# Kernel optimization log

Measured on AMD Instinct MI355X. Metric: run time of the kernel, lower is better.

## Reference

```python
import jax, jax.numpy as jnp
import numpy as np

D_QK = 32  # out_channels // 8


def conv1x1(x, w, b):
    # x: [B,C,H,W], w: [O,C], b: [O] -> [B,O,H,W]
    return jnp.einsum('bchw,oc->bohw', x, w) + b[None, :, None, None]


def setup_inputs() -> dict:
    key = jax.random.key(0)
    ks = jax.random.split(key, 10)
    B, C, H, W = 4, 256, 64, 64
    in_ch, out_ch, attn_ch = 512, 256, 256
    s_in = 1.0 / np.sqrt(in_ch)
    s_at = 1.0 / np.sqrt(attn_ch)
    return {
        'ef': jax.random.normal(ks[0], (B, C, H, W), jnp.float32),
        'sf': jax.random.normal(ks[1], (B, C, H, W), jnp.float32),
        'Attn': jax.random.normal(ks[2], (B, attn_ch, H, W), jnp.float32),
        'Qw': jax.random.uniform(ks[3], (D_QK, in_ch), jnp.float32, -s_in, s_in),
        'Qb': jax.random.uniform(ks[4], (D_QK,), jnp.float32, -s_in, s_in),
        'Kw': jax.random.uniform(ks[5], (D_QK, attn_ch), jnp.float32, -s_at, s_at),
        'Kb': jax.random.uniform(ks[6], (D_QK,), jnp.float32, -s_at, s_at),
        'Vw': jax.random.uniform(ks[7], (out_ch, in_ch), jnp.float32, -s_in, s_in),
        'Vb': jax.random.uniform(ks[8], (out_ch,), jnp.float32, -s_in, s_in),
        'gamma': jnp.ones((1,), jnp.float32) * 0.25,
    }


def reference(ef, sf, Attn, Qw, Qb, Kw, Kb, Vw, Vb, gamma):
    B, C, H, W = ef.shape
    N = H * W
    x = jnp.concatenate((ef, sf), axis=1)  # [B, 2C, H, W]
    q = conv1x1(x, Qw, Qb).reshape(B, D_QK, N)         # [B, d, N]
    k = conv1x1(Attn, Kw, Kb).reshape(B, D_QK, N)      # [B, d, N]
    # scores[b, m, n] = sum_d q[b, d, m] * k[b, d, n]  (no 1/sqrt(d) scale)
    scores = jnp.einsum('bdm,bdn->bmn', q, k)
    attn = jax.nn.softmax(scores, axis=-1)             # [B, N, N]
    v = conv1x1(x, Vw, Vb).reshape(B, C, N)            # [B, C, N]
    # out[b, c, m] = sum_n v[b, c, n] * attn[b, m, n]
    out = jnp.einsum('bcn,bmn->bcm', v, attn).reshape(B, C, H, W)
    return gamma[0] * out + ef
```

## Files before the change

kernel.cpp:

```cpp
#include <hip/hip_runtime.h>
#include <hip/hip_bf16.h>

typedef short bf16x8 __attribute__((ext_vector_type(8)));
typedef float f32x4 __attribute__((ext_vector_type(4)));

#define MFMA16(a, b, c) __builtin_amdgcn_mfma_f32_16x16x32_bf16(a, b, c, 0, 0, 0)

#define NB 4
#define NC 256
#define NSP 4096
#define LOG2E 1.4426950408889634f

__device__ __forceinline__ unsigned short f2bf(float f) {
    return (unsigned short)((__float_as_uint(f) + 0x8000u) >> 16);
}
__device__ __forceinline__ unsigned pk2bf(float hi, float lo) {
    return __builtin_amdgcn_perm(__float_as_uint(hi) + 0x8000u,
                                 __float_as_uint(lo) + 0x8000u, 0x07060302u);
}

__global__ __launch_bounds__(256) void prep_w(
    const float* __restrict__ Qw, const float* __restrict__ Kw,
    const float* __restrict__ Vw,
    unsigned short* __restrict__ Qwbf, unsigned short* __restrict__ Kwbf,
    unsigned short* __restrict__ Vwbf)
{
    int i = blockIdx.x * 256 + threadIdx.x;
    {
        const float4* vs = (const float4*)(Vw + (size_t)i * 8);
        float4 a = vs[0], c = vs[1];
        int4 st;
        st.x = (int)pk2bf(a.y, a.x); st.y = (int)pk2bf(a.w, a.z);
        st.z = (int)pk2bf(c.y, c.x); st.w = (int)pk2bf(c.w, c.z);
        *(int4*)(Vwbf + (size_t)i * 8) = st;
    }
    if (i < 2048) {
        const float4* qs = (const float4*)(Qw + (size_t)i * 8);
        float4 a = qs[0], c = qs[1];
        int4 st;
        st.x = (int)pk2bf(a.y, a.x); st.y = (int)pk2bf(a.w, a.z);
        st.z = (int)pk2bf(c.y, c.x); st.w = (int)pk2bf(c.w, c.z);
        *(int4*)(Qwbf + (size_t)i * 8) = st;
    }
    if (i < 1024) {
        const float4* ks = (const float4*)(Kw + (size_t)i * 8);
        float4 a = ks[0], c = ks[1];
        int4 st;
        st.x = (int)pk2bf(a.y, a.x); st.y = (int)pk2bf(a.w, a.z);
        st.z = (int)pk2bf(c.y, c.x); st.w = (int)pk2bf(c.w, c.z);
        *(int4*)(Kwbf + (size_t)i * 8) = st;
    }
}

__global__ __launch_bounds__(256, 2) void proj_qv(
    const float* __restrict__ ef, const float* __restrict__ sf,
    const unsigned short* __restrict__ Qwbf, const float* __restrict__ Qb,
    const unsigned short* __restrict__ Vwbf, const float* __restrict__ Vb,
    unsigned short* __restrict__ qws, unsigned short* __restrict__ vws)
{
    __shared__ __align__(16) unsigned short xt[2][32][72];

    int t = threadIdx.x;
    int w = t >> 6, lane = t & 63, quad = lane >> 4, l15 = lane & 15;
    int mt = blockIdx.x, b = blockIdx.y, m0 = mt * 32;
    int u = t & 7, v = t >> 3;
    int mi = w >> 1, oh = w & 1;

    float4 xA[8], xB[8];
#pragma unroll
    for (int c = 0; c < 8; ++c) {
        const float* sp = (c < 4 ? ef : sf) +
                          ((size_t)(b * NC) + (c & 3) * 64 + 2 * v) * NSP + m0 + u * 4;
        xA[c] = *(const float4*)sp;
        xB[c] = *(const float4*)(sp + NSP);
    }
    __builtin_amdgcn_sched_barrier(0);

    f32x4 zero = {0.f, 0.f, 0.f, 0.f};
    f32x4 acc[2][4];
#pragma unroll
    for (int m = 0; m < 2; ++m)
#pragma unroll
        for (int ot = 0; ot < 4; ++ot) acc[m][ot] = zero;
    f32x4 qacc = zero;

#pragma unroll
    for (int c = 0; c < 8; ++c) {
        unsigned* xw = (unsigned*)&xt[c & 1][u * 4][2 * v];
        xw[0]   = pk2bf(xB[c].x, xA[c].x);
        xw[36]  = pk2bf(xB[c].y, xA[c].y);
        xw[72]  = pk2bf(xB[c].z, xA[c].z);
        xw[108] = pk2bf(xB[c].w, xA[c].w);
        __syncthreads();
        int ci0 = c * 64;
#pragma unroll
        for (int ks = 0; ks < 2; ++ks) {
            bf16x8 a0 = *(const bf16x8*)&xt[c & 1][l15][ks * 32 + quad * 8];
            bf16x8 a1 = *(const bf16x8*)&xt[c & 1][16 + l15][ks * 32 + quad * 8];
            bf16x8 bq = *(const bf16x8*)(Qwbf + (size_t)(oh * 16 + l15) * 512 + ci0 + ks * 32 + quad * 8);
            qacc = MFMA16(mi ? a1 : a0, bq, qacc);
#pragma unroll
            for (int ot = 0; ot < 4; ++ot) {
                bf16x8 bv = *(const bf16x8*)(Vwbf + (size_t)(w * 64 + ot * 16 + l15) * 512 + ci0 + ks * 32 + quad * 8);
                acc[0][ot] = MFMA16(a0, bv, acc[0][ot]);
                acc[1][ot] = MFMA16(a1, bv, acc[1][ot]);
            }
        }
    }

#pragma unroll
    for (int ot = 0; ot < 4; ++ot) {
        int ch = w * 64 + ot * 16 + l15;
        float bias = Vb[ch];
        unsigned* vp = (unsigned*)(vws + ((size_t)((b * 128 + mt) * 256 + ch)) * 32);
#pragma unroll
        for (int r = 0; r < 4; ++r)
            vp[quad * 4 + r] = pk2bf(acc[1][ot][r] + bias, acc[0][ot][r] + bias);
    }
    {
        int o = oh * 16 + l15;
        float bb = Qb[o];
#pragma unroll
        for (int r = 0; r < 4; ++r) {
            int m = m0 + mi * 16 + quad * 4 + r;
            qws[((size_t)(b * NSP) + m) * 32 + o] = f2bf((qacc[r] + bb) * LOG2E);
        }
    }
}

__global__ __launch_bounds__(256, 2) void proj_k(
    const float* __restrict__ attn,
    const unsigned short* __restrict__ Kwbf, const float* __restrict__ Kb,
    unsigned short* __restrict__ kws)
{
    __shared__ __align__(16) unsigned short xt[2][32][72];

    int t = threadIdx.x;
    int w = t >> 6, lane = t & 63, quad = lane >> 4, l15 = lane & 15;
    int mt = blockIdx.x, b = blockIdx.y, m0 = mt * 32;
    int u = t & 7, v = t >> 3;
    int mi = w >> 1, oh = w & 1;

    float4 xA[4], xB[4];
#pragma unroll
    for (int c = 0; c < 4; ++c) {
        const float* sp = attn + ((size_t)(b * NC) + c * 64 + 2 * v) * NSP + m0 + u * 4;
        xA[c] = *(const float4*)sp;
        xB[c] = *(const float4*)(sp + NSP);
    }
    __builtin_amdgcn_sched_barrier(0);

    f32x4 acc = {0.f, 0.f, 0.f, 0.f};

#pragma unroll
    for (int c = 0; c < 4; ++c) {
        unsigned* xw = (unsigned*)&xt[c & 1][u * 4][2 * v];
        xw[0]   = pk2bf(xB[c].x, xA[c].x);
        xw[36]  = pk2bf(xB[c].y, xA[c].y);
        xw[72]  = pk2bf(xB[c].z, xA[c].z);
        xw[108] = pk2bf(xB[c].w, xA[c].w);
        __syncthreads();
        int ci0 = c * 64;
#pragma unroll
        for (int ks = 0; ks < 2; ++ks) {
            bf16x8 a  = *(const bf16x8*)&xt[c & 1][mi * 16 + l15][ks * 32 + quad * 8];
            bf16x8 bk = *(const bf16x8*)(Kwbf + (size_t)(oh * 16 + l15) * 256 + ci0 + ks * 32 + quad * 8);
            acc = MFMA16(a, bk, acc);
        }
    }

    int o = oh * 16 + l15;
    float bb = Kb[o];
#pragma unroll
    for (int r = 0; r < 4; ++r) {
        int m = m0 + mi * 16 + quad * 4 + r;
        kws[((size_t)(b * NSP) + m) * 32 + o] = f2bf(acc[r] + bb);
    }
}

__global__ __launch_bounds__(512, 4) void attention(
    const unsigned short* __restrict__ qws, const unsigned short* __restrict__ kws,
    const unsigned short* __restrict__ vws, const float* __restrict__ ef,
    const float* __restrict__ gamma, float* __restrict__ out)
{
    __shared__ __align__(16) unsigned short Plds[2][2][32 * 72];
    __shared__ __align__(16) float denl[2][2][32];

    int t = threadIdx.x;
    int g = t >> 8, tl = t & 255;
    int w = tl >> 6, lane = tl & 63, quad = lane >> 4, l15 = lane & 15;
    int qh = w & 1, kh = w >> 1;
    int b = blockIdx.x >> 7, m0 = (blockIdx.x & 127) << 5;

    const unsigned short* kbase = kws + (size_t)(b * NSP) * 32;
    const unsigned short* vbase = vws + (size_t)(b * 128) * 8192;

    bf16x8 qf = *(const bf16x8*)(qws + ((size_t)(b * NSP) + m0 + qh * 16 + l15) * 32 + quad * 8);

    f32x4 zero = {0.f, 0.f, 0.f, 0.f};
    f32x4 acc[2][4];
#pragma unroll
    for (int i = 0; i < 2; ++i)
#pragma unroll
        for (int j = 0; j < 4; ++j) acc[i][j] = zero;
    float lp0 = 0.f, lp1 = 0.f, lp2 = 0.f, lp3 = 0.f;

    for (int it = 0; it < 32; ++it) {
        int buf = it & 1;
        int T = g * 64 + 2 * it;

        bf16x8 kf0 = *(const bf16x8*)(kbase + (size_t)((T + kh) * 32 + l15) * 32 + quad * 8);
        bf16x8 kf1 = *(const bf16x8*)(kbase + (size_t)((T + kh) * 32 + 16 + l15) * 32 + quad * 8);
        f32x4 s0 = MFMA16(qf, kf0, zero);
        f32x4 s1 = MFMA16(qf, kf1, zero);

        float e0[4], e1[4];
#pragma unroll
        for (int r = 0; r < 4; ++r) {
            e0[r] = __builtin_amdgcn_exp2f(s0[r]);
            e1[r] = __builtin_amdgcn_exp2f(s1[r]);
        }
        lp0 += e0[0] + e1[0];
        lp1 += e0[1] + e1[1];
        lp2 += e0[2] + e1[2];
        lp3 += e0[3] + e1[3];

        unsigned short* pd = &Plds[g][buf][(qh * 16 + quad * 4) * 72 + kh * 32 + 2 * l15];
#pragma unroll
        for (int r = 0; r < 4; ++r)
            *(unsigned*)(pd + r * 72) = pk2bf(e1[r], e0[r]);

        __syncthreads();

        bf16x8 vf[2][4];
#pragma unroll
        for (int h = 0; h < 2; ++h)
#pragma unroll
            for (int cc = 0; cc < 4; ++cc)
                vf[h][cc] = *(const bf16x8*)(vbase + (size_t)(T + h) * 8192 + (w * 64 + cc * 16 + l15) * 32 + quad * 8);

#pragma unroll
        for (int h = 0; h < 2; ++h) {
            bf16x8 pa0 = *(const bf16x8*)&Plds[g][buf][(0  + l15) * 72 + h * 32 + quad * 8];
            bf16x8 pa1 = *(const bf16x8*)&Plds[g][buf][(16 + l15) * 72 + h * 32 + quad * 8];
#pragma unroll
            for (int cc = 0; cc < 4; ++cc) {
                acc[0][cc] = MFMA16(pa0, vf[h][cc], acc[0][cc]);
                acc[1][cc] = MFMA16(pa1, vf[h][cc], acc[1][cc]);
            }
        }
    }

    lp0 += __shfl_xor(lp0, 1); lp0 += __shfl_xor(lp0, 2); lp0 += __shfl_xor(lp0, 4); lp0 += __shfl_xor(lp0, 8);
    lp1 += __shfl_xor(lp1, 1); lp1 += __shfl_xor(lp1, 2); lp1 += __shfl_xor(lp1, 4); lp1 += __shfl_xor(lp1, 8);
    lp2 += __shfl_xor(lp2, 1); lp2 += __shfl_xor(lp2, 2); lp2 += __shfl_xor(lp2, 4); lp2 += __shfl_xor(lp2, 8);
    lp3 += __shfl_xor(lp3, 1); lp3 += __shfl_xor(lp3, 2); lp3 += __shfl_xor(lp3, 4); lp3 += __shfl_xor(lp3, 8);
    if (l15 == 0) {
        int base = qh * 16 + quad * 4;
        denl[g][kh][base + 0] = lp0; denl[g][kh][base + 1] = lp1;
        denl[g][kh][base + 2] = lp2; denl[g][kh][base + 3] = lp3;
    }
    __syncthreads();

    float (*mrgO)[36] = (float (*)[36])&Plds[0][0][0];
    float gam = gamma[0];

#pragma unroll
    for (int half = 0; half < 2; ++half) {
        if (g == 1) {
#pragma unroll
            for (int qc2 = 0; qc2 < 2; ++qc2)
#pragma unroll
                for (int c2 = 0; c2 < 2; ++c2)
                    *(f32x4*)&mrgO[w * 32 + c2 * 16 + l15][qc2 * 16 + quad * 4] = acc[qc2][half * 2 + c2];
        }
        __syncthreads();
        if (g == 0) {
#pragma unroll
            for (int qc2 = 0; qc2 < 2; ++qc2) {
                int qb = qc2 * 16 + quad * 4;
                float4 d00 = *(const float4*)&denl[0][0][qb];
                float4 d01 = *(const float4*)&denl[0][1][qb];
                float4 d10 = *(const float4*)&denl[1][0][qb];
                float4 d11 = *(const float4*)&denl[1][1][qb];
                float r0 = gam / ((d00.x + d01.x) + (d10.x + d11.x));
                float r1 = gam / ((d00.y + d01.y) + (d10.y + d11.y));
                float r2 = gam / ((d00.z + d01.z) + (d10.z + d11.z));
                float r3 = gam / ((d00.w + d01.w) + (d10.w + d11.w));
#pragma unroll
                for (int c2 = 0; c2 < 2; ++c2) {
                    int cc = half * 2 + c2;
                    int ch = w * 64 + cc * 16 + l15;
                    f32x4 part = *(const f32x4*)&mrgO[w * 32 + c2 * 16 + l15][qb];
                    size_t off = ((size_t)(b * NC + ch)) * NSP + m0 + qb;
                    float4 e = *(const float4*)(ef + off);
                    float4 o;
                    o.x = (acc[qc2][cc][0] + part[0]) * r0 + e.x;
                    o.y = (acc[qc2][cc][1] + part[1]) * r1 + e.y;
                    o.z = (acc[qc2][cc][2] + part[2]) * r2 + e.z;
                    o.w = (acc[qc2][cc][3] + part[3]) * r3 + e.w;
                    *(float4*)(out + off) = o;
                }
            }
        }
        __syncthreads();
    }
}

extern "C" void kernel_launch(void* const* d_in, const int* in_sizes, int n_in,
                              void* d_out, int out_size, void* d_ws, size_t ws_size,
                              hipStream_t stream) {
    const float* ef    = (const float*)d_in[0];
    const float* sf    = (const float*)d_in[1];
    const float* attn  = (const float*)d_in[2];
    const float* Qw    = (const float*)d_in[3];
    const float* Qb    = (const float*)d_in[4];
    const float* Kw    = (const float*)d_in[5];
    const float* Kb    = (const float*)d_in[6];
    const float* Vw    = (const float*)d_in[7];
    const float* Vb    = (const float*)d_in[8];
    const float* gamma = (const float*)d_in[9];
    float* out = (float*)d_out;

    unsigned short* qws  = (unsigned short*)d_ws;
    unsigned short* kws  = qws + (size_t)4 * 4096 * 32;
    unsigned short* vws  = kws + (size_t)4 * 4096 * 32;
    unsigned short* Qwbf = vws + (size_t)4 * 128 * 256 * 32;
    unsigned short* Kwbf = Qwbf + 32 * 512;
    unsigned short* Vwbf = Kwbf + 32 * 256;

    hipLaunchKernelGGL(prep_w, dim3(64), dim3(256), 0, stream,
                       Qw, Kw, Vw, Qwbf, Kwbf, Vwbf);
    hipLaunchKernelGGL(proj_qv, dim3(128, 4), dim3(256), 0, stream,
                       ef, sf, Qwbf, Qb, Vwbf, Vb, qws, vws);
    hipLaunchKernelGGL(proj_k, dim3(128, 4), dim3(256), 0, stream,
                       attn, Kwbf, Kb, kws);
    hipLaunchKernelGGL(attention, dim3(512), dim3(512), 0, stream,
                       qws, kws, vws, ef, gamma, out);
}
```

Before: 211.5 us.

## Keep softmax P in registers by transposing score MFMA, removing LDS round-trip

The attention kernel computes scores as K·Q so that each lane's exp outputs directly form the bf16 A-operand for the P·V MFMA, removing the per-iteration LDS write, __syncthreads and reload of P. Each wave now owns 16 query rows and all 256 channels (16 accumulators), the block covers 64 queries, the grid is halved to 256 blocks, and the key range is split across two wave groups merged through a larger LDS buffer at the end. This removes intra-loop barriers but raises register pressure (launch bounds lowered to 2 blocks per CU) and leaves fewer blocks to fill the GPU.

```diff
diff --git a/kernel.cpp b/kernel.cpp
--- a/kernel.cpp
+++ b/kernel.cpp
@@ -178,41 +178,36 @@
     }
 }
 
-__global__ __launch_bounds__(512, 4) void attention(
+__global__ __launch_bounds__(512, 2) void attention(
     const unsigned short* __restrict__ qws, const unsigned short* __restrict__ kws,
     const unsigned short* __restrict__ vws, const float* __restrict__ ef,
     const float* __restrict__ gamma, float* __restrict__ out)
 {
-    __shared__ __align__(16) unsigned short Plds[2][2][32 * 72];
-    __shared__ __align__(16) float denl[2][2][32];
+    __shared__ __align__(16) float mrg[256][68];
+    __shared__ __align__(16) float denl[2][4][16];
 
     int t = threadIdx.x;
-    int g = t >> 8, tl = t & 255;
-    int w = tl >> 6, lane = tl & 63, quad = lane >> 4, l15 = lane & 15;
-    int qh = w & 1, kh = w >> 1;
-    int b = blockIdx.x >> 7, m0 = (blockIdx.x & 127) << 5;
+    int w = t >> 6, lane = t & 63, quad = lane >> 4, l15 = lane & 15;
+    int qt = w & 3, g = w >> 2;
+    int b = blockIdx.x >> 6, m0 = (blockIdx.x & 63) << 6;
 
     const unsigned short* kbase = kws + (size_t)(b * NSP) * 32;
     const unsigned short* vbase = vws + (size_t)(b * 128) * 8192;
 
-    bf16x8 qf = *(const bf16x8*)(qws + ((size_t)(b * NSP) + m0 + qh * 16 + l15) * 32 + quad * 8);
+    bf16x8 qf = *(const bf16x8*)(qws + ((size_t)(b * NSP) + m0 + qt * 16 + l15) * 32 + quad * 8);
 
     f32x4 zero = {0.f, 0.f, 0.f, 0.f};
-    f32x4 acc[2][4];
-#pragma unroll
-    for (int i = 0; i < 2; ++i)
-#pragma unroll
-        for (int j = 0; j < 4; ++j) acc[i][j] = zero;
-    float lp0 = 0.f, lp1 = 0.f, lp2 = 0.f, lp3 = 0.f;
-
-    for (int it = 0; it < 32; ++it) {
-        int buf = it & 1;
-        int T = g * 64 + 2 * it;
-
-        bf16x8 kf0 = *(const bf16x8*)(kbase + (size_t)((T + kh) * 32 + l15) * 32 + quad * 8);
-        bf16x8 kf1 = *(const bf16x8*)(kbase + (size_t)((T + kh) * 32 + 16 + l15) * 32 + quad * 8);
-        f32x4 s0 = MFMA16(qf, kf0, zero);
-        f32x4 s1 = MFMA16(qf, kf1, zero);
+    f32x4 acc[16];
+#pragma unroll
+    for (int cc = 0; cc < 16; ++cc) acc[cc] = zero;
+    float lp = 0.f;
+
+    for (int tt = 0; tt < 64; ++tt) {
+        int T = g * 64 + tt;
+        bf16x8 kf0 = *(const bf16x8*)(kbase + (size_t)(T * 32 + l15) * 32 + quad * 8);
+        bf16x8 kf1 = *(const bf16x8*)(kbase + (size_t)(T * 32 + 16 + l15) * 32 + quad * 8);
+        f32x4 s0 = MFMA16(kf0, qf, zero);
+        f32x4 s1 = MFMA16(kf1, qf, zero);
 
         float e0[4], e1[4];
 #pragma unroll
@@ -220,90 +215,53 @@
             e0[r] = __builtin_amdgcn_exp2f(s0[r]);
             e1[r] = __builtin_amdgcn_exp2f(s1[r]);
         }
-        lp0 += e0[0] + e1[0];
-        lp1 += e0[1] + e1[1];
-        lp2 += e0[2] + e1[2];
-        lp3 += e0[3] + e1[3];
-
-        unsigned short* pd = &Plds[g][buf][(qh * 16 + quad * 4) * 72 + kh * 32 + 2 * l15];
-#pragma unroll
-        for (int r = 0; r < 4; ++r)
-            *(unsigned*)(pd + r * 72) = pk2bf(e1[r], e0[r]);
-
-        __syncthreads();
-
-        bf16x8 vf[2][4];
-#pragma unroll
-        for (int h = 0; h < 2; ++h)
-#pragma unroll
-            for (int cc = 0; cc < 4; ++cc)
-                vf[h][cc] = *(const bf16x8*)(vbase + (size_t)(T + h) * 8192 + (w * 64 + cc * 16 + l15) * 32 + quad * 8);
-
-#pragma unroll
-        for (int h = 0; h < 2; ++h) {
-            bf16x8 pa0 = *(const bf16x8*)&Plds[g][buf][(0  + l15) * 72 + h * 32 + quad * 8];
-            bf16x8 pa1 = *(const bf16x8*)&Plds[g][buf][(16 + l15) * 72 + h * 32 + quad * 8];
-#pragma unroll
-            for (int cc = 0; cc < 4; ++cc) {
-                acc[0][cc] = MFMA16(pa0, vf[h][cc], acc[0][cc]);
-                acc[1][cc] = MFMA16(pa1, vf[h][cc], acc[1][cc]);
-            }
-        }
-    }
-
-    lp0 += __shfl_xor(lp0, 1); lp0 += __shfl_xor(lp0, 2); lp0 += __shfl_xor(lp0, 4); lp0 += __shfl_xor(lp0, 8);
-    lp1 += __shfl_xor(lp1, 1); lp1 += __shfl_xor(lp1, 2); lp1 += __shfl_xor(lp1, 4); lp1 += __shfl_xor(lp1, 8);
-    lp2 += __shfl_xor(lp2, 1); lp2 += __shfl_xor(lp2, 2); lp2 += __shfl_xor(lp2, 4); lp2 += __shfl_xor(lp2, 8);
-    lp3 += __shfl_xor(lp3, 1); lp3 += __shfl_xor(lp3, 2); lp3 += __shfl_xor(lp3, 4); lp3 += __shfl_xor(lp3, 8);
-    if (l15 == 0) {
-        int base = qh * 16 + quad * 4;
-        denl[g][kh][base + 0] = lp0; denl[g][kh][base + 1] = lp1;
-        denl[g][kh][base + 2] = lp2; denl[g][kh][base + 3] = lp3;
+        lp += (e0[0] + e1[0]) + (e0[1] + e1[1]) + (e0[2] + e1[2]) + (e0[3] + e1[3]);
+
+        int4 pai;
+        pai.x = (int)pk2bf(e1[0], e0[0]);
+        pai.y = (int)pk2bf(e1[1], e0[1]);
+        pai.z = (int)pk2bf(e1[2], e0[2]);
+        pai.w = (int)pk2bf(e1[3], e0[3]);
+        bf16x8 pa = *(bf16x8*)&pai;
+
+        const unsigned short* vt = vbase + (size_t)T * 8192;
+#pragma unroll
+        for (int cc = 0; cc < 16; ++cc) {
+            bf16x8 vf = *(const bf16x8*)(vt + (cc * 16 + l15) * 32 + quad * 8);
+            acc[cc] = MFMA16(pa, vf, acc[cc]);
+        }
+    }
+
+    lp += __shfl_xor(lp, 16);
+    lp += __shfl_xor(lp, 32);
+    if (lane < 16) denl[g][qt][lane] = lp;
+
+    if (g == 1) {
+#pragma unroll
+        for (int cc = 0; cc < 16; ++cc)
+            *(f32x4*)&mrg[cc * 16 + l15][qt * 16 + quad * 4] = acc[cc];
     }
     __syncthreads();
 
-    float (*mrgO)[36] = (float (*)[36])&Plds[0][0][0];
-    float gam = gamma[0];
-
-#pragma unroll
-    for (int half = 0; half < 2; ++half) {
-        if (g == 1) {
-#pragma unroll
-            for (int qc2 = 0; qc2 < 2; ++qc2)
-#pragma unroll
-                for (int c2 = 0; c2 < 2; ++c2)
-                    *(f32x4*)&mrgO[w * 32 + c2 * 16 + l15][qc2 * 16 + quad * 4] = acc[qc2][half * 2 + c2];
-        }
-        __syncthreads();
-        if (g == 0) {
-#pragma unroll
-            for (int qc2 = 0; qc2 < 2; ++qc2) {
-                int qb = qc2 * 16 + quad * 4;
-                float4 d00 = *(const float4*)&denl[0][0][qb];
-                float4 d01 = *(const float4*)&denl[0][1][qb];
-                float4 d10 = *(const float4*)&denl[1][0][qb];
-                float4 d11 = *(const float4*)&denl[1][1][qb];
-                float r0 = gam / ((d00.x + d01.x) + (d10.x + d11.x));
-                float r1 = gam / ((d00.y + d01.y) + (d10.y + d11.y));
-                float r2 = gam / ((d00.z + d01.z) + (d10.z + d11.z));
-                float r3 = gam / ((d00.w + d01.w) + (d10.w + d11.w));
-#pragma unroll
-                for (int c2 = 0; c2 < 2; ++c2) {
-                    int cc = half * 2 + c2;
-                    int ch = w * 64 + cc * 16 + l15;
-                    f32x4 part = *(const f32x4*)&mrgO[w * 32 + c2 * 16 + l15][qb];
-                    size_t off = ((size_t)(b * NC + ch)) * NSP + m0 + qb;
-                    float4 e = *(const float4*)(ef + off);
-                    float4 o;
-                    o.x = (acc[qc2][cc][0] + part[0]) * r0 + e.x;
-                    o.y = (acc[qc2][cc][1] + part[1]) * r1 + e.y;
-                    o.z = (acc[qc2][cc][2] + part[2]) * r2 + e.z;
-                    o.w = (acc[qc2][cc][3] + part[3]) * r3 + e.w;
-                    *(float4*)(out + off) = o;
-                }
-            }
-        }
-        __syncthreads();
+    if (g == 0) {
+        float gam = gamma[0];
+        float4 d0 = *(const float4*)&denl[0][qt][quad * 4];
+        float4 d1 = *(const float4*)&denl[1][qt][quad * 4];
+        float r0 = gam / (d0.x + d1.x), r1 = gam / (d0.y + d1.y);
+        float r2 = gam / (d0.z + d1.z), r3 = gam / (d0.w + d1.w);
+#pragma unroll
+        for (int cc = 0; cc < 16; ++cc) {
+            int ch = cc * 16 + l15;
+            f32x4 part = *(const f32x4*)&mrg[ch][qt * 16 + quad * 4];
+            size_t off = ((size_t)(b * NC + ch)) * NSP + m0 + qt * 16 + quad * 4;
+            float4 e = *(const float4*)(ef + off);
+            float4 o;
+            o.x = (acc[cc][0] + part[0]) * r0 + e.x;
+            o.y = (acc[cc][1] + part[1]) * r1 + e.y;
+            o.z = (acc[cc][2] + part[2]) * r2 + e.z;
+            o.w = (acc[cc][3] + part[3]) * r3 + e.w;
+            *(float4*)(out + off) = o;
+        }
     }
 }
 
@@ -335,6 +293,6 @@
                        ef, sf, Qwbf, Qb, Vwbf, Vb, qws, vws);
     hipLaunchKernelGGL(proj_k, dim3(128, 4), dim3(256), 0, stream,
                        attn, Kwbf, Kb, kws);
-    hipLaunchKernelGGL(attention, dim3(512), dim3(512), 0, stream,
+    hipLaunchKernelGGL(attention, dim3(256), dim3(512), 0, stream,
                        qws, kws, vws, ef, gamma, out);
 }
```

Result: slower. 269.8 us (+27.6%).
